# Optimization experiments

Measured on AMD Instinct MI355X. Metric: run time of the kernel, lower is better.

## Reference

```python
import jax, jax.numpy as jnp
import numpy as np

L, N, E = 2048, 2, 1024
H = 16                      # num_heads
DH = E // H                 # head_dim = 64
SCALE = DH ** -0.5
NEG = -10000.0


def setup_inputs() -> dict:
    key = jax.random.key(0)
    ks = jax.random.split(key, 9)
    s = 0.02
    return {
        "query": jax.random.normal(ks[0], (L, N, E), jnp.float32),
        "q_proj": jax.random.normal(ks[1], (E, E), jnp.float32) * s,
        "q_bias": jax.random.normal(ks[2], (E,), jnp.float32) * s,
        "k_proj": jax.random.normal(ks[3], (E, E), jnp.float32) * s,
        "k_bias": jax.random.normal(ks[4], (E,), jnp.float32) * s,
        "v_proj": jax.random.normal(ks[5], (E, E), jnp.float32) * s,
        "v_bias": jax.random.normal(ks[6], (E,), jnp.float32) * s,
        "out_proj": jax.random.normal(ks[7], (E, E), jnp.float32) * s,
        "out_bias": jax.random.normal(ks[8], (E,), jnp.float32) * s,
    }


def reference(query, q_proj, q_bias, k_proj, k_bias, v_proj, v_bias, out_proj, out_bias):
    # query: [L, N, E]; projections act as F.linear: x @ W.T + b
    q = query @ q_proj.T + q_bias
    k = query @ k_proj.T + k_bias
    v = query @ v_proj.T + v_bias
    # [L, N*H, DH] -> [N*H, L, DH]
    q = q.reshape(L, N * H, DH).transpose(1, 0, 2) * SCALE
    k = k.reshape(L, N * H, DH).transpose(1, 0, 2)
    v = v.reshape(L, N * H, DH).transpose(1, 0, 2)
    attn = jnp.einsum('bqd,bkd->bqk', q, k)  # [N*H, L, L]
    causal = jnp.tril(jnp.ones((L, L), jnp.float32)) < 0.5  # True above diagonal
    attn = jnp.where(causal[None, :, :], NEG, attn)
    attn = jax.nn.softmax(attn, axis=-1)
    # dropout_p = 0.0 in training mode -> identity
    out = jnp.einsum('bqk,bkd->bqd', attn, v)  # [N*H, L, DH]
    out = out.transpose(1, 0, 2).reshape(L, N, H * DH)
    return out @ out_proj.T + out_bias
```

## Files before the change

### kernel.cpp

```cpp
#include <hip/hip_runtime.h>
#include <stdint.h>

typedef __attribute__((ext_vector_type(8)))  short          bf16x8;
typedef __attribute__((ext_vector_type(4)))  float          f32x4;
typedef __attribute__((ext_vector_type(16))) float          f32x16;
typedef __attribute__((ext_vector_type(4)))  unsigned int   u32x4;
typedef __attribute__((ext_vector_type(4)))  unsigned short u16x4;

#define SCALE_LOG2E 0.180336880f

static __device__ __forceinline__ unsigned short f2bf(float x) {
  union { float f; unsigned int u; } c; c.f = x;
  unsigned int r = c.u + 0x7fffu + ((c.u >> 16) & 1u);
  return (unsigned short)(r >> 16);
}

static __device__ __forceinline__ unsigned int cvt_pk_bf16(float lo, float hi) {
  unsigned int r;
  asm("v_cvt_pk_bf16_f32 %0, %1, %2" : "=v"(r) : "v"(lo), "v"(hi));
  return r;
}

static __device__ __forceinline__ void stage16(const unsigned short* g, unsigned short* l) {
  __builtin_amdgcn_global_load_lds(
      (const __attribute__((address_space(1))) unsigned int*)g,
      (__attribute__((address_space(3)))       unsigned int*)l, 16, 0, 0);
}

__global__ __launch_bounds__(256) void cvt_f32_bf16(const float* __restrict__ src,
                                                    unsigned short* __restrict__ dst, int n) {
  int i = (blockIdx.x * 256 + threadIdx.x) * 4;
  if (i < n) {
    float4 v = *(const float4*)(src + i);
    u16x4 o; o.x = f2bf(v.x); o.y = f2bf(v.y); o.z = f2bf(v.z); o.w = f2bf(v.w);
    *(u16x4*)(dst + i) = o;
  }
}

__global__ __launch_bounds__(256) void cvt_w4(const float* __restrict__ wq, const float* __restrict__ wk,
                                              const float* __restrict__ wv, const float* __restrict__ wo,
                                              unsigned short* __restrict__ dst) {
  const int z = blockIdx.y;
  const float* src = z == 0 ? wq : (z == 1 ? wk : (z == 2 ? wv : wo));
  int i = (blockIdx.x * 256 + threadIdx.x) * 4;
  float4 v = *(const float4*)(src + i);
  u16x4 o; o.x = f2bf(v.x); o.y = f2bf(v.y); o.z = f2bf(v.z); o.w = f2bf(v.w);
  *(u16x4*)(dst + (size_t)z * 1048576 + i) = o;
}

__device__ __forceinline__ void gemm_tile_core(const unsigned short* __restrict__ A,
                                               const unsigned short* __restrict__ B,
                                               int bi, int bj, f32x4 (&acc)[4][4]) {
  __shared__ unsigned short As[128 * 32];
  __shared__ unsigned short Bs[128 * 32];
  const int t = threadIdx.x, w = t >> 6, l = t & 63;
  const int l15 = l & 15, l4 = l >> 4;
  const int wm = w >> 1, wn = w & 1;
  const int srow = l >> 2, scol = (l & 3) * 8;

#pragma unroll
  for (int m = 0; m < 4; m++)
#pragma unroll
    for (int n = 0; n < 4; n++)
#pragma unroll
      for (int r = 0; r < 4; r++) acc[m][n][r] = 0.f;

  const int koff = 8 * l4;
  for (int k0 = 0; k0 < 1024; k0 += 32) {
    stage16(A + (size_t)(bi * 128 + w * 16 + srow) * 1024 + k0 + scol, (unsigned short*)As + w * 512);
    stage16(A + (size_t)(bi * 128 + (w + 4) * 16 + srow) * 1024 + k0 + scol, (unsigned short*)As + (w + 4) * 512);
    stage16(B + (size_t)(bj * 128 + w * 16 + srow) * 1024 + k0 + scol, (unsigned short*)Bs + w * 512);
    stage16(B + (size_t)(bj * 128 + (w + 4) * 16 + srow) * 1024 + k0 + scol, (unsigned short*)Bs + (w + 4) * 512);
    __syncthreads();

    bf16x8 af[4], bfr[4];
#pragma unroll
    for (int m = 0; m < 4; m++) af[m]  = *(const bf16x8*)(As + (wm * 64 + m * 16 + l15) * 32 + koff);
#pragma unroll
    for (int n = 0; n < 4; n++) bfr[n] = *(const bf16x8*)(Bs + (wn * 64 + n * 16 + l15) * 32 + koff);
#pragma unroll
    for (int m = 0; m < 4; m++)
#pragma unroll
      for (int n = 0; n < 4; n++)
        acc[m][n] = __builtin_amdgcn_mfma_f32_16x16x32_bf16(af[m], bfr[n], acc[m][n], 0, 0, 0);
    __syncthreads();
  }
}

__global__ __launch_bounds__(256) void gemm_qkv(
    const unsigned short* __restrict__ X,
    const unsigned short* __restrict__ Wq, const unsigned short* __restrict__ Wk,
    const unsigned short* __restrict__ Wv,
    const float* __restrict__ bq, const float* __restrict__ bk, const float* __restrict__ bv,
    unsigned short* __restrict__ Qf, unsigned short* __restrict__ Kf, unsigned short* __restrict__ Vf) {
  const int mode = blockIdx.z;
  const unsigned short* W = mode == 0 ? Wq : (mode == 1 ? Wk : Wv);
  const float* bias = mode == 0 ? bq : (mode == 1 ? bk : bv);
  f32x4 acc[4][4];
  gemm_tile_core(X, W, blockIdx.y, blockIdx.x, acc);

  const int t = threadIdx.x, w = t >> 6, l = t & 63;
  const int l15 = l & 15, l4 = l >> 4;
  const int wm = w >> 1, wn = w & 1;
  const int i0 = blockIdx.y * 128 + wm * 64 + 4 * l4;
  const int j0 = blockIdx.x * 128 + wn * 64 + l15;
#pragma unroll
  for (int m = 0; m < 4; m++)
#pragma unroll
    for (int n = 0; n < 4; n++) {
      const int j = j0 + n * 16;
      const float bv_ = bias[j];
      const int h = j >> 6, d = j & 63;
#pragma unroll
      for (int r = 0; r < 4; r++) {
        const int i = i0 + m * 16 + r;
        const int n_ = i & 1, ll = i >> 1;
        const int b = n_ * 16 + h;
        const int kt = ll >> 5, l31k = ll & 31;
        float v = acc[m][n][r] + bv_;
        if (mode == 0) {
          const int lane = l31k + 32 * ((d >> 3) & 1);
          Qf[((size_t)(b * 64 + kt) * 4 + (d >> 4)) * 512 + lane * 8 + (d & 7)] = f2bf(v * SCALE_LOG2E);
        } else if (mode == 1) {
          const int lane = l31k + 32 * ((d >> 3) & 1);
          Kf[((size_t)(b * 64 + kt) * 4 + (d >> 4)) * 512 + lane * 8 + (d & 7)] = f2bf(v);
        } else {
          const int j2 = 2 * (d >> 5) + ((l31k >> 4) & 1);
          const int lane = (d & 31) + 32 * ((l31k >> 3) & 1);
          Vf[((size_t)(b * 64 + kt) * 4 + j2) * 512 + lane * 8 + (l31k & 7)] = f2bf(v);
        }
      }
    }
}

__global__ __launch_bounds__(256) void gemm_out(
    const unsigned short* __restrict__ X2, const unsigned short* __restrict__ Wo,
    const float* __restrict__ bias, float* __restrict__ out) {
  f32x4 acc[4][4];
  gemm_tile_core(X2, Wo, blockIdx.y, blockIdx.x, acc);
  const int t = threadIdx.x, w = t >> 6, l = t & 63;
  const int l15 = l & 15, l4 = l >> 4;
  const int wm = w >> 1, wn = w & 1;
  const int i0 = blockIdx.y * 128 + wm * 64 + 4 * l4;
  const int j0 = blockIdx.x * 128 + wn * 64 + l15;
#pragma unroll
  for (int m = 0; m < 4; m++)
#pragma unroll
    for (int n = 0; n < 4; n++) {
      const int j = j0 + n * 16;
      const float bv_ = bias[j];
#pragma unroll
      for (int r = 0; r < 4; r++)
        out[(size_t)(i0 + m * 16 + r) * 1024 + j] = acc[m][n][r] + bv_;
    }
}

__global__ __launch_bounds__(256) void attn_kernel(
    const unsigned short* __restrict__ Qf, const unsigned short* __restrict__ Kf,
    const unsigned short* __restrict__ Vf, unsigned short* __restrict__ X2) {
  __shared__ float po[4 * 64 * 17];
  __shared__ float mbuf[4][32];
  __shared__ float lbuf[4][32];

  const unsigned id = blockIdx.x;
  const int s_ = id >> 3;
  const int b = (id & 7) * 4 + (s_ & 3);
  const int t = 63 - (s_ >> 2);

  const int w = threadIdx.x >> 6, l = threadIdx.x & 63;
  const int l31 = l & 31, g = l >> 5;

  const unsigned short* qp = Qf + ((size_t)(b * 64 + t) * 4) * 512 + l * 8;
  bf16x8 qf[4];
#pragma unroll
  for (int s = 0; s < 4; s++) qf[s] = *(const bf16x8*)(qp + s * 512);

  f32x16 o0, o1;
#pragma unroll
  for (int r = 0; r < 16; r++) { o0[r] = 0.f; o1[r] = 0.f; }
  float m_run = -1e30f, lsum = 0.f;

  const unsigned short* kb = Kf + (size_t)b * 131072;
  const unsigned short* vb = Vf + (size_t)b * 131072;

  int kt = w;
  bf16x8 kf[4], vf[4];
  if (kt <= t) {
    const unsigned short* kp = kb + kt * 2048 + l * 8;
    const unsigned short* vp = vb + kt * 2048 + l * 8;
#pragma unroll
    for (int s = 0; s < 4; s++) { kf[s] = *(const bf16x8*)(kp + s * 512); vf[s] = *(const bf16x8*)(vp + s * 512); }
  }

  for (; kt <= t; kt += 4) {
    const int ktn = (kt + 4 <= t) ? kt + 4 : t;
    const unsigned short* kp = kb + ktn * 2048 + l * 8;
    const unsigned short* vp = vb + ktn * 2048 + l * 8;
    bf16x8 kn[4], vn[4];
#pragma unroll
    for (int s = 0; s < 4; s++) { kn[s] = *(const bf16x8*)(kp + s * 512); vn[s] = *(const bf16x8*)(vp + s * 512); }
    __builtin_amdgcn_sched_barrier(0);

    f32x16 sa;
#pragma unroll
    for (int r = 0; r < 16; r++) sa[r] = 0.f;
#pragma unroll
    for (int s = 0; s < 4; s++)
      sa = __builtin_amdgcn_mfma_f32_32x32x16_bf16(kf[s], qf[s], sa, 0, 0, 0);

    float p[16];
#pragma unroll
    for (int r = 0; r < 16; r++) p[r] = sa[r];
    if (kt == t) {
#pragma unroll
      for (int r = 0; r < 16; r++) {
        const int kvloc = (r & 3) + 8 * (r >> 2) + 4 * g;
        p[r] = (kvloc <= l31) ? p[r] : -30000.f;
      }
    }
    float x0 = fmaxf(p[0], p[1]),  x1 = fmaxf(p[2], p[3]),  x2 = fmaxf(p[4], p[5]),  x3 = fmaxf(p[6], p[7]);
    float x4 = fmaxf(p[8], p[9]),  x5 = fmaxf(p[10], p[11]), x6 = fmaxf(p[12], p[13]), x7 = fmaxf(p[14], p[15]);
    x0 = fmaxf(x0, x1); x2 = fmaxf(x2, x3); x4 = fmaxf(x4, x5); x6 = fmaxf(x6, x7);
    const float mloc = fmaxf(fmaxf(x0, x2), fmaxf(x4, x6));
    const float mtile = fmaxf(mloc, __shfl_xor(mloc, 32, 64));
    if (__any(mtile > m_run + 8.f)) {
      const float mnew = fmaxf(m_run, mtile);
      const float sc = exp2f(m_run - mnew);
      m_run = mnew;
      lsum *= sc;
#pragma unroll
      for (int r = 0; r < 16; r++) { o0[r] *= sc; o1[r] *= sc; }
    }
#pragma unroll
    for (int r = 0; r < 16; r++) p[r] = exp2f(p[r] - m_run);
    float a0 = p[0] + p[1],  a1 = p[2] + p[3],  a2 = p[4] + p[5],  a3 = p[6] + p[7];
    float a4 = p[8] + p[9],  a5 = p[10] + p[11], a6 = p[12] + p[13], a7 = p[14] + p[15];
    a0 += a1; a2 += a3; a4 += a5; a6 += a7;
    lsum += (a0 + a2) + (a4 + a6);

    unsigned int u[8], pu[8];
#pragma unroll
    for (int i = 0; i < 8; i++) u[i] = cvt_pk_bf16(p[2 * i], p[2 * i + 1]);
#pragma unroll
    for (int i = 0; i < 8; i++) pu[i] = (unsigned int)__shfl_xor((int)u[i], 32, 64);
    u32x4 B0, B1;
    B0.x = g ? pu[2] : u[0];  B0.y = g ? pu[3] : u[1];
    B0.z = g ? u[2] : pu[0];  B0.w = g ? u[3] : pu[1];
    B1.x = g ? pu[6] : u[4];  B1.y = g ? pu[7] : u[5];
    B1.z = g ? u[6] : pu[4];  B1.w = g ? u[7] : pu[5];
    const bf16x8 pb0 = __builtin_bit_cast(bf16x8, B0);
    const bf16x8 pb1 = __builtin_bit_cast(bf16x8, B1);

    o0 = __builtin_amdgcn_mfma_f32_32x32x16_bf16(vf[0], pb0, o0, 0, 0, 0);
    o0 = __builtin_amdgcn_mfma_f32_32x32x16_bf16(vf[1], pb1, o0, 0, 0, 0);
    o1 = __builtin_amdgcn_mfma_f32_32x32x16_bf16(vf[2], pb0, o1, 0, 0, 0);
    o1 = __builtin_amdgcn_mfma_f32_32x32x16_bf16(vf[3], pb1, o1, 0, 0, 0);

#pragma unroll
    for (int s = 0; s < 4; s++) { kf[s] = kn[s]; vf[s] = vn[s]; }
  }

  const float lsum_full = lsum + __shfl_xor(lsum, 32, 64);
  float* mypo = po + (w * 64 + l) * 17;
#pragma unroll
  for (int r = 0; r < 16; r++) mypo[r] = o0[r];
  if (l < 32) { mbuf[w][l] = m_run; lbuf[w][l] = lsum_full; }
  __syncthreads();

  float ms[4];
#pragma unroll
  for (int s = 0; s < 4; s++) ms[s] = mbuf[s][l31];
  const float mt = fmaxf(fmaxf(ms[0], ms[1]), fmaxf(ms[2], ms[3]));
  float scf[4]; float lt = 0.f;
#pragma unroll
  for (int s = 0; s < 4; s++) { scf[s] = exp2f(ms[s] - mt); lt += scf[s] * lbuf[s][l31]; }
  const float inv = 1.f / lt;

  float c0[4] = {0.f, 0.f, 0.f, 0.f}, c1[4] = {0.f, 0.f, 0.f, 0.f};
#pragma unroll
  for (int s = 0; s < 4; s++) {
    const float* pp = po + (s * 64 + l) * 17 + w * 4;
#pragma unroll
    for (int j = 0; j < 4; j++) c0[j] += scf[s] * pp[j];
  }
  __syncthreads();
#pragma unroll
  for (int r = 0; r < 16; r++) mypo[r] = o1[r];
  __syncthreads();
#pragma unroll
  for (int s = 0; s < 4; s++) {
    const float* pp = po + (s * 64 + l) * 17 + w * 4;
#pragma unroll
    for (int j = 0; j < 4; j++) c1[j] += scf[s] * pp[j];
  }

  const int n_ = b >> 4, h = b & 15;
  const int q0 = t * 32;
  unsigned short* orow = X2 + ((size_t)((q0 + l31) * 2 + n_)) * 1024 + h * 64;
#pragma unroll
  for (int j = 0; j < 4; j++) {
    const int d = j + 8 * w + 4 * g;
    orow[d]      = f2bf(c0[j] * inv);
    orow[32 + d] = f2bf(c1[j] * inv);
  }
}

extern "C" void kernel_launch(void* const* d_in, const int* in_sizes, int n_in,
                              void* d_out, int out_size, void* d_ws, size_t ws_size,
                              hipStream_t stream) {
  const float* query    = (const float*)d_in[0];
  const float* q_proj   = (const float*)d_in[1];
  const float* q_bias   = (const float*)d_in[2];
  const float* k_proj   = (const float*)d_in[3];
  const float* k_bias   = (const float*)d_in[4];
  const float* v_proj   = (const float*)d_in[5];
  const float* v_bias   = (const float*)d_in[6];
  const float* out_proj = (const float*)d_in[7];
  const float* out_bias = (const float*)d_in[8];
  float* out = (float*)d_out;

  char* ws = (char*)d_ws;
  unsigned short* Xq = (unsigned short*)(ws);
  unsigned short* Wq = (unsigned short*)(ws + (8u << 20));
  unsigned short* Qf = (unsigned short*)(ws + (16u << 20));
  unsigned short* Kf = (unsigned short*)(ws + (24u << 20));
  unsigned short* Vf = (unsigned short*)(ws + (32u << 20));
  unsigned short* X2 = (unsigned short*)(ws + (40u << 20));
  unsigned short* Wk = Wq + 1048576;
  unsigned short* Wv = Wq + 2097152;
  unsigned short* Wo = Wq + 3145728;

  cvt_f32_bf16<<<4096, 256, 0, stream>>>(query, Xq, 4194304);
  cvt_w4<<<dim3(1024, 4), 256, 0, stream>>>(q_proj, k_proj, v_proj, out_proj, Wq);

  gemm_qkv<<<dim3(8, 32, 3), 256, 0, stream>>>(Xq, Wq, Wk, Wv, q_bias, k_bias, v_bias, Qf, Kf, Vf);
  attn_kernel<<<2048, 256, 0, stream>>>(Qf, Kf, Vf, X2);
  gemm_out<<<dim3(8, 32), 256, 0, stream>>>(X2, Wo, out_bias, out);
}
```

Baseline: 120.1 us.

## Pair complementary causal query tiles per block to share K/V loads

Each attention block now processes two query tiles, p and 63-p, so every block does the same amount of causal work. The K/V fragments loaded for the longer tile are reused for the shorter one, which cuts global K/V traffic and evens out the load across the grid. The grid is halved to 1024 blocks and launch_bounds asks for 2 blocks per CU. The cost is higher register pressure from two sets of accumulators, and an epilogue that now takes more LDS passes and barriers.

```diff
diff --git a/kernel.cpp b/kernel.cpp
--- a/kernel.cpp
+++ b/kernel.cpp
@@ -155,154 +155,205 @@
     }
 }
 
-__global__ __launch_bounds__(256) void attn_kernel(
+static __device__ __forceinline__ void tile_step(
+    const f32x16& sa, bool diag, int l31, int g,
+    float& m_run, float& lsum, f32x16& o0, f32x16& o1, const bf16x8 (&vf)[4]) {
+  float e[16];
+#pragma unroll
+  for (int r = 0; r < 16; r++) e[r] = sa[r];
+  if (diag) {
+#pragma unroll
+    for (int r = 0; r < 16; r++) {
+      const int kvloc = (r & 3) + 8 * (r >> 2) + 4 * g;
+      e[r] = (kvloc <= l31) ? e[r] : -30000.f;
+    }
+  }
+  float a0 = fmaxf(fmaxf(e[0], e[1]), e[2]);
+  float a1 = fmaxf(fmaxf(e[3], e[4]), e[5]);
+  float a2 = fmaxf(fmaxf(e[6], e[7]), e[8]);
+  float a3 = fmaxf(fmaxf(e[9], e[10]), e[11]);
+  float a4 = fmaxf(fmaxf(e[12], e[13]), e[14]);
+  const float mloc = fmaxf(fmaxf(fmaxf(a0, a1), fmaxf(a2, a3)), fmaxf(a4, e[15]));
+  const float mtile = fmaxf(mloc, __shfl_xor(mloc, 32, 64));
+  if (__any(mtile > m_run + 8.f)) {
+    const float mnew = fmaxf(m_run, mtile);
+    const float sc = exp2f(m_run - mnew);
+    m_run = mnew; lsum *= sc;
+#pragma unroll
+    for (int r = 0; r < 16; r++) { o0[r] *= sc; o1[r] *= sc; }
+  }
+#pragma unroll
+  for (int r = 0; r < 16; r++) e[r] = exp2f(e[r] - m_run);
+  const float s0 = (e[0] + e[1]) + (e[2] + e[3]),   s1 = (e[4] + e[5]) + (e[6] + e[7]);
+  const float s2 = (e[8] + e[9]) + (e[10] + e[11]), s3 = (e[12] + e[13]) + (e[14] + e[15]);
+  lsum += (s0 + s1) + (s2 + s3);
+
+  unsigned int u[8], pu[8];
+#pragma unroll
+  for (int i = 0; i < 8; i++) u[i] = cvt_pk_bf16(e[2 * i], e[2 * i + 1]);
+#pragma unroll
+  for (int i = 0; i < 8; i++) pu[i] = (unsigned int)__shfl_xor((int)u[i], 32, 64);
+  u32x4 B0, B1;
+  B0.x = g ? pu[2] : u[0];  B0.y = g ? pu[3] : u[1];
+  B0.z = g ? u[2] : pu[0];  B0.w = g ? u[3] : pu[1];
+  B1.x = g ? pu[6] : u[4];  B1.y = g ? pu[7] : u[5];
+  B1.z = g ? u[6] : pu[4];  B1.w = g ? u[7] : pu[5];
+  const bf16x8 pb0 = __builtin_bit_cast(bf16x8, B0);
+  const bf16x8 pb1 = __builtin_bit_cast(bf16x8, B1);
+  o0 = __builtin_amdgcn_mfma_f32_32x32x16_bf16(vf[0], pb0, o0, 0, 0, 0);
+  o0 = __builtin_amdgcn_mfma_f32_32x32x16_bf16(vf[1], pb1, o0, 0, 0, 0);
+  o1 = __builtin_amdgcn_mfma_f32_32x32x16_bf16(vf[2], pb0, o1, 0, 0, 0);
+  o1 = __builtin_amdgcn_mfma_f32_32x32x16_bf16(vf[3], pb1, o1, 0, 0, 0);
+}
+
+__global__ __launch_bounds__(256, 2) void attn_kernel(
     const unsigned short* __restrict__ Qf, const unsigned short* __restrict__ Kf,
     const unsigned short* __restrict__ Vf, unsigned short* __restrict__ X2) {
   __shared__ float po[4 * 64 * 17];
-  __shared__ float mbuf[4][32];
-  __shared__ float lbuf[4][32];
+  __shared__ float mb[2][4][32];
+  __shared__ float lb[2][4][32];
 
   const unsigned id = blockIdx.x;
-  const int s_ = id >> 3;
-  const int b = (id & 7) * 4 + (s_ & 3);
-  const int t = 63 - (s_ >> 2);
+  const int b = (id & 7) * 4 + ((id >> 3) & 3);
+  const int p = id >> 5;
+  const int t2 = 63 - p;
 
   const int w = threadIdx.x >> 6, l = threadIdx.x & 63;
   const int l31 = l & 31, g = l >> 5;
 
-  const unsigned short* qp = Qf + ((size_t)(b * 64 + t) * 4) * 512 + l * 8;
-  bf16x8 qf[4];
-#pragma unroll
-  for (int s = 0; s < 4; s++) qf[s] = *(const bf16x8*)(qp + s * 512);
-
-  f32x16 o0, o1;
-#pragma unroll
-  for (int r = 0; r < 16; r++) { o0[r] = 0.f; o1[r] = 0.f; }
-  float m_run = -1e30f, lsum = 0.f;
-
-  const unsigned short* kb = Kf + (size_t)b * 131072;
-  const unsigned short* vb = Vf + (size_t)b * 131072;
-
-  int kt = w;
+  const unsigned short* qp1 = Qf + ((size_t)(b * 64 + p) * 4) * 512 + l * 8;
+  const unsigned short* qp2 = Qf + ((size_t)(b * 64 + t2) * 4) * 512 + l * 8;
+  bf16x8 qf1[4], qf2[4];
+#pragma unroll
+  for (int s = 0; s < 4; s++) { qf1[s] = *(const bf16x8*)(qp1 + s * 512); qf2[s] = *(const bf16x8*)(qp2 + s * 512); }
+
+  f32x16 z;
+#pragma unroll
+  for (int r = 0; r < 16; r++) z[r] = 0.f;
+  f32x16 o10 = z, o11 = z, o20 = z, o21 = z;
+  float m1 = -1e30f, ls1 = 0.f, m2 = -1e30f, ls2 = 0.f;
+
+  const unsigned short* kb_ = Kf + (size_t)b * 131072;
+  const unsigned short* vb_ = Vf + (size_t)b * 131072;
+
   bf16x8 kf[4], vf[4];
-  if (kt <= t) {
-    const unsigned short* kp = kb + kt * 2048 + l * 8;
-    const unsigned short* vp = vb + kt * 2048 + l * 8;
+  {
+    const unsigned short* kp = kb_ + w * 2048 + l * 8;
+    const unsigned short* vp = vb_ + w * 2048 + l * 8;
 #pragma unroll
     for (int s = 0; s < 4; s++) { kf[s] = *(const bf16x8*)(kp + s * 512); vf[s] = *(const bf16x8*)(vp + s * 512); }
   }
 
-  for (; kt <= t; kt += 4) {
-    const int ktn = (kt + 4 <= t) ? kt + 4 : t;
-    const unsigned short* kp = kb + ktn * 2048 + l * 8;
-    const unsigned short* vp = vb + ktn * 2048 + l * 8;
+  for (int kt = w; kt <= t2; kt += 4) {
+    const int ktn = (kt + 4 <= t2) ? kt + 4 : t2;
+    const unsigned short* kp = kb_ + ktn * 2048 + l * 8;
+    const unsigned short* vp = vb_ + ktn * 2048 + l * 8;
     bf16x8 kn[4], vn[4];
 #pragma unroll
     for (int s = 0; s < 4; s++) { kn[s] = *(const bf16x8*)(kp + s * 512); vn[s] = *(const bf16x8*)(vp + s * 512); }
     __builtin_amdgcn_sched_barrier(0);
 
-    f32x16 sa;
-#pragma unroll
-    for (int r = 0; r < 16; r++) sa[r] = 0.f;
-#pragma unroll
-    for (int s = 0; s < 4; s++)
-      sa = __builtin_amdgcn_mfma_f32_32x32x16_bf16(kf[s], qf[s], sa, 0, 0, 0);
-
-    float p[16];
-#pragma unroll
-    for (int r = 0; r < 16; r++) p[r] = sa[r];
-    if (kt == t) {
-#pragma unroll
-      for (int r = 0; r < 16; r++) {
-        const int kvloc = (r & 3) + 8 * (r >> 2) + 4 * g;
-        p[r] = (kvloc <= l31) ? p[r] : -30000.f;
-      }
+    f32x16 sa = __builtin_amdgcn_mfma_f32_32x32x16_bf16(kf[0], qf2[0], z, 0, 0, 0);
+#pragma unroll
+    for (int s = 1; s < 4; s++) sa = __builtin_amdgcn_mfma_f32_32x32x16_bf16(kf[s], qf2[s], sa, 0, 0, 0);
+    tile_step(sa, kt == t2, l31, g, m2, ls2, o20, o21, vf);
+
+    if (kt <= p) {
+      f32x16 sb = __builtin_amdgcn_mfma_f32_32x32x16_bf16(kf[0], qf1[0], z, 0, 0, 0);
+#pragma unroll
+      for (int s = 1; s < 4; s++) sb = __builtin_amdgcn_mfma_f32_32x32x16_bf16(kf[s], qf1[s], sb, 0, 0, 0);
+      tile_step(sb, kt == p, l31, g, m1, ls1, o10, o11, vf);
     }
-    float x0 = fmaxf(p[0], p[1]),  x1 = fmaxf(p[2], p[3]),  x2 = fmaxf(p[4], p[5]),  x3 = fmaxf(p[6], p[7]);
-    float x4 = fmaxf(p[8], p[9]),  x5 = fmaxf(p[10], p[11]), x6 = fmaxf(p[12], p[13]), x7 = fmaxf(p[14], p[15]);
-    x0 = fmaxf(x0, x1); x2 = fmaxf(x2, x3); x4 = fmaxf(x4, x5); x6 = fmaxf(x6, x7);
-    const float mloc = fmaxf(fmaxf(x0, x2), fmaxf(x4, x6));
-    const float mtile = fmaxf(mloc, __shfl_xor(mloc, 32, 64));
-    if (__any(mtile > m_run + 8.f)) {
-      const float mnew = fmaxf(m_run, mtile);
-      const float sc = exp2f(m_run - mnew);
-      m_run = mnew;
-      lsum *= sc;
-#pragma unroll
-      for (int r = 0; r < 16; r++) { o0[r] *= sc; o1[r] *= sc; }
-    }
-#pragma unroll
-    for (int r = 0; r < 16; r++) p[r] = exp2f(p[r] - m_run);
-    float a0 = p[0] + p[1],  a1 = p[2] + p[3],  a2 = p[4] + p[5],  a3 = p[6] + p[7];
-    float a4 = p[8] + p[9],  a5 = p[10] + p[11], a6 = p[12] + p[13], a7 = p[14] + p[15];
-    a0 += a1; a2 += a3; a4 += a5; a6 += a7;
-    lsum += (a0 + a2) + (a4 + a6);
-
-    unsigned int u[8], pu[8];
-#pragma unroll
-    for (int i = 0; i < 8; i++) u[i] = cvt_pk_bf16(p[2 * i], p[2 * i + 1]);
-#pragma unroll
-    for (int i = 0; i < 8; i++) pu[i] = (unsigned int)__shfl_xor((int)u[i], 32, 64);
-    u32x4 B0, B1;
-    B0.x = g ? pu[2] : u[0];  B0.y = g ? pu[3] : u[1];
-    B0.z = g ? u[2] : pu[0];  B0.w = g ? u[3] : pu[1];
-    B1.x = g ? pu[6] : u[4];  B1.y = g ? pu[7] : u[5];
-    B1.z = g ? u[6] : pu[4];  B1.w = g ? u[7] : pu[5];
-    const bf16x8 pb0 = __builtin_bit_cast(bf16x8, B0);
-    const bf16x8 pb1 = __builtin_bit_cast(bf16x8, B1);
-
-    o0 = __builtin_amdgcn_mfma_f32_32x32x16_bf16(vf[0], pb0, o0, 0, 0, 0);
-    o0 = __builtin_amdgcn_mfma_f32_32x32x16_bf16(vf[1], pb1, o0, 0, 0, 0);
-    o1 = __builtin_amdgcn_mfma_f32_32x32x16_bf16(vf[2], pb0, o1, 0, 0, 0);
-    o1 = __builtin_amdgcn_mfma_f32_32x32x16_bf16(vf[3], pb1, o1, 0, 0, 0);
 
 #pragma unroll
     for (int s = 0; s < 4; s++) { kf[s] = kn[s]; vf[s] = vn[s]; }
   }
 
-  const float lsum_full = lsum + __shfl_xor(lsum, 32, 64);
+  const float ls1f = ls1 + __shfl_xor(ls1, 32, 64);
+  const float ls2f = ls2 + __shfl_xor(ls2, 32, 64);
   float* mypo = po + (w * 64 + l) * 17;
-#pragma unroll
-  for (int r = 0; r < 16; r++) mypo[r] = o0[r];
-  if (l < 32) { mbuf[w][l] = m_run; lbuf[w][l] = lsum_full; }
-  __syncthreads();
-
-  float ms[4];
-#pragma unroll
-  for (int s = 0; s < 4; s++) ms[s] = mbuf[s][l31];
-  const float mt = fmaxf(fmaxf(ms[0], ms[1]), fmaxf(ms[2], ms[3]));
-  float scf[4]; float lt = 0.f;
-#pragma unroll
-  for (int s = 0; s < 4; s++) { scf[s] = exp2f(ms[s] - mt); lt += scf[s] * lbuf[s][l31]; }
-  const float inv = 1.f / lt;
-
-  float c0[4] = {0.f, 0.f, 0.f, 0.f}, c1[4] = {0.f, 0.f, 0.f, 0.f};
+  if (l < 32) { mb[0][w][l] = m1; lb[0][w][l] = ls1f; mb[1][w][l] = m2; lb[1][w][l] = ls2f; }
+#pragma unroll
+  for (int r = 0; r < 16; r++) mypo[r] = o10[r];
+  __syncthreads();
+
+  float scf1[4], scf2[4], inv1, inv2;
+  {
+    float ms0 = mb[0][0][l31], ms1 = mb[0][1][l31], ms2 = mb[0][2][l31], ms3 = mb[0][3][l31];
+    const float mt = fmaxf(fmaxf(ms0, ms1), fmaxf(ms2, ms3));
+    scf1[0] = exp2f(ms0 - mt); scf1[1] = exp2f(ms1 - mt); scf1[2] = exp2f(ms2 - mt); scf1[3] = exp2f(ms3 - mt);
+    float lt = scf1[0] * lb[0][0][l31] + scf1[1] * lb[0][1][l31] + scf1[2] * lb[0][2][l31] + scf1[3] * lb[0][3][l31];
+    inv1 = 1.f / lt;
+  }
+  {
+    float ms0 = mb[1][0][l31], ms1 = mb[1][1][l31], ms2 = mb[1][2][l31], ms3 = mb[1][3][l31];
+    const float mt = fmaxf(fmaxf(ms0, ms1), fmaxf(ms2, ms3));
+    scf2[0] = exp2f(ms0 - mt); scf2[1] = exp2f(ms1 - mt); scf2[2] = exp2f(ms2 - mt); scf2[3] = exp2f(ms3 - mt);
+    float lt = scf2[0] * lb[1][0][l31] + scf2[1] * lb[1][1][l31] + scf2[2] * lb[1][2][l31] + scf2[3] * lb[1][3][l31];
+    inv2 = 1.f / lt;
+  }
+
+  const int n_ = b >> 4, h = b & 15;
+  unsigned short* orow1 = X2 + ((size_t)((32 * p + l31) * 2 + n_)) * 1024 + h * 64;
+  unsigned short* orow2 = X2 + ((size_t)((32 * t2 + l31) * 2 + n_)) * 1024 + h * 64;
+  const int dbase = 8 * w + 4 * g;
+  float c[4];
+
+#pragma unroll
+  for (int j = 0; j < 4; j++) c[j] = 0.f;
 #pragma unroll
   for (int s = 0; s < 4; s++) {
     const float* pp = po + (s * 64 + l) * 17 + w * 4;
 #pragma unroll
-    for (int j = 0; j < 4; j++) c0[j] += scf[s] * pp[j];
-  }
-  __syncthreads();
-#pragma unroll
-  for (int r = 0; r < 16; r++) mypo[r] = o1[r];
-  __syncthreads();
+    for (int j = 0; j < 4; j++) c[j] += scf1[s] * pp[j];
+  }
+#pragma unroll
+  for (int j = 0; j < 4; j++) orow1[dbase + j] = f2bf(c[j] * inv1);
+  __syncthreads();
+
+#pragma unroll
+  for (int r = 0; r < 16; r++) mypo[r] = o11[r];
+  __syncthreads();
+#pragma unroll
+  for (int j = 0; j < 4; j++) c[j] = 0.f;
 #pragma unroll
   for (int s = 0; s < 4; s++) {
     const float* pp = po + (s * 64 + l) * 17 + w * 4;
 #pragma unroll
-    for (int j = 0; j < 4; j++) c1[j] += scf[s] * pp[j];
-  }
-
-  const int n_ = b >> 4, h = b & 15;
-  const int q0 = t * 32;
-  unsigned short* orow = X2 + ((size_t)((q0 + l31) * 2 + n_)) * 1024 + h * 64;
-#pragma unroll
-  for (int j = 0; j < 4; j++) {
-    const int d = j + 8 * w + 4 * g;
-    orow[d]      = f2bf(c0[j] * inv);
-    orow[32 + d] = f2bf(c1[j] * inv);
-  }
+    for (int j = 0; j < 4; j++) c[j] += scf1[s] * pp[j];
+  }
+#pragma unroll
+  for (int j = 0; j < 4; j++) orow1[32 + dbase + j] = f2bf(c[j] * inv1);
+  __syncthreads();
+
+#pragma unroll
+  for (int r = 0; r < 16; r++) mypo[r] = o20[r];
+  __syncthreads();
+#pragma unroll
+  for (int j = 0; j < 4; j++) c[j] = 0.f;
+#pragma unroll
+  for (int s = 0; s < 4; s++) {
+    const float* pp = po + (s * 64 + l) * 17 + w * 4;
+#pragma unroll
+    for (int j = 0; j < 4; j++) c[j] += scf2[s] * pp[j];
+  }
+#pragma unroll
+  for (int j = 0; j < 4; j++) orow2[dbase + j] = f2bf(c[j] * inv2);
+  __syncthreads();
+
+#pragma unroll
+  for (int r = 0; r < 16; r++) mypo[r] = o21[r];
+  __syncthreads();
+#pragma unroll
+  for (int j = 0; j < 4; j++) c[j] = 0.f;
+#pragma unroll
+  for (int s = 0; s < 4; s++) {
+    const float* pp = po + (s * 64 + l) * 17 + w * 4;
+#pragma unroll
+    for (int j = 0; j < 4; j++) c[j] += scf2[s] * pp[j];
+  }
+#pragma unroll
+  for (int j = 0; j < 4; j++) orow2[32 + dbase + j] = f2bf(c[j] * inv2);
 }
 
 extern "C" void kernel_launch(void* const* d_in, const int* in_sizes, int n_in,
@@ -334,6 +385,6 @@
   cvt_w4<<<dim3(1024, 4), 256, 0, stream>>>(q_proj, k_proj, v_proj, out_proj, Wq);
 
   gemm_qkv<<<dim3(8, 32, 3), 256, 0, stream>>>(Xq, Wq, Wk, Wv, q_bias, k_bias, v_bias, Qf, Kf, Vf);
-  attn_kernel<<<2048, 256, 0, stream>>>(Qf, Kf, Vf, X2);
+  attn_kernel<<<1024, 256, 0, stream>>>(Qf, Kf, Vf, X2);
   gemm_out<<<dim3(8, 32), 256, 0, stream>>>(X2, Wo, out_bias, out);
 }
```

New measurement: 114.3 us. -4.8%, faster.
